# Performance work log

Hardware: AMD Instinct MI355X
Metric: run time of the kernel (lower is better)

Reference implementation:

```python
import jax, jax.numpy as jnp
import numpy as np

DROPOUT_P = 0.5  # used as an additive constant in the normalizers, not as dropout
N = 384


def setup_inputs() -> dict:
    key = jax.random.key(0)
    k1, k2 = jax.random.split(key)
    inp = jax.random.uniform(k1, (N, N, N), dtype=jnp.float32)
    w = jax.random.uniform(k2, (N, N, N), dtype=jnp.float32)
    return {"input": inp, "w": w}


def reference(input, w):
    # e[i,j,l] = sum_k input[i,j,k] * w[l,k,j]
    e = jnp.einsum('ijk,lkj->ijl', input, w)
    # k (normalized by input row-sums) is dead code in the original forward;
    # only q and v feed the output, so we skip it.
    v = e  # second identical einsum in the source
    s_in = input.sum(axis=-1, keepdims=True)          # [N, N, 1]
    # einsum('ijk,ijl->ijl', input, w) == (sum_k input) * w
    q = s_in * w
    q = q / (DROPOUT_P + w.sum(axis=-1, keepdims=True))
    # causal mask: strict upper triangle set to -inf, broadcast over batch
    mask = jnp.triu(jnp.full((N, N), -jnp.inf, dtype=q.dtype), k=1)  # [N, N]
    attn = jax.nn.softmax(q + mask[None, :, :], axis=-1)              # [N, N, N]
    return jnp.matmul(attn, v)
```

## Files before the change

### kernel.cpp

```cpp
#include <hip/hip_runtime.h>
#include <hip/hip_bf16.h>


#define N 384
#define N2 (N * N)
#define BK 64
static const size_t N3 = (size_t)N * N * N;

typedef __attribute__((ext_vector_type(8))) short s16x8;
typedef __attribute__((ext_vector_type(4))) float f32x4;

#define AS1 __attribute__((address_space(1)))
#define AS3 __attribute__((address_space(3)))
__device__ __forceinline__ void gll16(const void* g, void* l) {
    __builtin_amdgcn_global_load_lds((const AS1 unsigned int*)g,
                                     (AS3 unsigned int*)l, 16, 0, 0);
}

__device__ __forceinline__ unsigned short f32_to_bf16(float f) {
    unsigned int u = __float_as_uint(f);
    u += 0x7FFFu + ((u >> 16) & 1u);
    return (unsigned short)(u >> 16);
}
__device__ __forceinline__ float bf16_to_f32(unsigned short h) {
    return __uint_as_float((unsigned int)h << 16);
}
__device__ __forceinline__ unsigned int pk2(float a, float b) {
    return (unsigned int)f32_to_bf16(a) | ((unsigned int)f32_to_bf16(b) << 16);
}

__global__ __launch_bounds__(256) void kT(const float* __restrict__ w,
                                          unsigned short* __restrict__ wt) {
    __shared__ unsigned short tile[64][68];
    const int r0 = blockIdx.x * 64;
    const int j0 = blockIdx.y * 64;
    const int tx = threadIdx.x & 63;
    const int ty = threadIdx.x >> 6;
#pragma unroll
    for (int p = 0; p < 16; ++p) {
        const int r = ty * 16 + p;
        tile[r][tx] = f32_to_bf16(w[(size_t)(r0 + r) * N + j0 + tx]);
    }
    __syncthreads();
#pragma unroll
    for (int p = 0; p < 16; ++p) {
        const int jj = ty * 16 + p;
        wt[(size_t)(j0 + jj) * N2 + r0 + tx] = tile[tx][jj];
    }
}

__global__ __launch_bounds__(256, 4) void k_e2(const float* __restrict__ in,
                                               const unsigned short* __restrict__ wt,
                                               unsigned short* __restrict__ e,
                                               float* __restrict__ rs) {
    __shared__ union {
        struct { unsigned short A[64 * 64]; unsigned short B[192 * 64]; } s;
        unsigned short C[64 * 200];
    } sm;

    const int lin = blockIdx.x;
    const int swz = (lin & 7) * 576 + (lin >> 3);
    const int j   = swz / 12;
    const int sub = swz % 12;
    const int i0  = (sub >> 1) * 64;
    const int l0  = (sub & 1) * 192;

    const int t = threadIdx.x, lane = t & 63, wv = t >> 6;
    const int fr = lane & 15, fx = lane >> 4;

    const int ra = t >> 2, ca = (t & 3) * 2;
    const float* Ab = in + (size_t)(i0 + ra) * N2 + (size_t)j * N + ca * 8;
    unsigned short* AsW0 = sm.s.A + ra * 64 + (((ca + 0) ^ (ra & 7)) * 8);
    unsigned short* AsW1 = sm.s.A + ra * 64 + (((ca + 1) ^ (ra & 7)) * 8);

    const unsigned short* Wj = wt + (size_t)j * N2 + (size_t)l0 * N;
    const int rb_off = lane >> 3;
    const int p8     = lane & 7;

    f32x4 acc[4][3];
#pragma unroll
    for (int m = 0; m < 4; ++m)
#pragma unroll
        for (int n = 0; n < 3; ++n) acc[m][n] = (f32x4){0.f, 0.f, 0.f, 0.f};

    float rsum = 0.f;

    float4 va[4];
    va[0] = *(const float4*)(Ab);
    va[1] = *(const float4*)(Ab + 4);
    va[2] = *(const float4*)(Ab + 8);
    va[3] = *(const float4*)(Ab + 12);

    for (int k0 = 0; k0 < N; k0 += BK) {
        __syncthreads();
        {
            rsum += (va[0].x + va[0].y + va[0].z + va[0].w) +
                    (va[1].x + va[1].y + va[1].z + va[1].w) +
                    (va[2].x + va[2].y + va[2].z + va[2].w) +
                    (va[3].x + va[3].y + va[3].z + va[3].w);
            uint4 a0, a1;
            a0.x = pk2(va[0].x, va[0].y); a0.y = pk2(va[0].z, va[0].w);
            a0.z = pk2(va[1].x, va[1].y); a0.w = pk2(va[1].z, va[1].w);
            a1.x = pk2(va[2].x, va[2].y); a1.y = pk2(va[2].z, va[2].w);
            a1.z = pk2(va[3].x, va[3].y); a1.w = pk2(va[3].z, va[3].w);
            *(uint4*)AsW0 = a0;
            *(uint4*)AsW1 = a1;
        }
#pragma unroll
        for (int itb = 0; itb < 6; ++itb) {
            const int rb = wv * 48 + itb * 8 + rb_off;
            const int sc = p8 ^ (rb & 7);
            gll16(Wj + (size_t)rb * N + k0 + sc * 8,
                  sm.s.B + (wv * 48 + itb * 8) * 64);
        }
        if (k0 + BK < N) {
            const float* An = Ab + k0 + BK;
            va[0] = *(const float4*)(An);
            va[1] = *(const float4*)(An + 4);
            va[2] = *(const float4*)(An + 8);
            va[3] = *(const float4*)(An + 12);
        }
        __syncthreads();
#pragma unroll
        for (int kk = 0; kk < 2; ++kk) {
            s16x8 af[4], bf[3];
#pragma unroll
            for (int m = 0; m < 4; ++m) {
                const int row = m * 16 + fr;
                const int x   = (kk * 4 + fx) ^ (row & 7);
                af[m] = *(const s16x8*)(sm.s.A + row * 64 + x * 8);
            }
#pragma unroll
            for (int n = 0; n < 3; ++n) {
                const int row = wv * 48 + n * 16 + fr;
                const int x   = (kk * 4 + fx) ^ (row & 7);
                bf[n] = *(const s16x8*)(sm.s.B + row * 64 + x * 8);
            }
#pragma unroll
            for (int m = 0; m < 4; ++m)
#pragma unroll
                for (int n = 0; n < 3; ++n)
                    acc[m][n] = __builtin_amdgcn_mfma_f32_16x16x32_bf16(
                        af[m], bf[n], acc[m][n], 0, 0, 0);
        }
    }

    rsum += __shfl_xor(rsum, 1, 64);
    rsum += __shfl_xor(rsum, 2, 64);
    if (rs != nullptr && l0 == 0 && (t & 3) == 0)
        rs[(size_t)(i0 + ra) * N + j] = rsum;

    __syncthreads();
#pragma unroll
    for (int m = 0; m < 4; ++m)
#pragma unroll
        for (int n = 0; n < 3; ++n)
#pragma unroll
            for (int r = 0; r < 4; ++r)
                sm.C[(m * 16 + fx * 4 + r) * 200 + wv * 48 + n * 16 + fr] =
                    f32_to_bf16(acc[m][n][r]);
    __syncthreads();
#pragma unroll
    for (int it = 0; it < 6; ++it) {
        const int cid = it * 256 + t;
        const int row = cid / 24;
        const int c   = cid % 24;
        *(uint4*)(e + (size_t)(i0 + row) * N2 + (size_t)j * N + l0 + c * 8) =
            *(const uint4*)&sm.C[row * 200 + c * 8];
    }
}

__global__ __launch_bounds__(256) void k_eT(const unsigned short* __restrict__ e,
                                            unsigned short* __restrict__ et) {
    __shared__ unsigned short tile[64][68];
    const int m0 = blockIdx.x * 64, l0 = blockIdx.y * 64;
    const size_t ib = (size_t)blockIdx.z * N2;
    const int t  = threadIdx.x;
    const int c4 = (t & 15) * 4, r = t >> 4;
#pragma unroll
    for (int p = 0; p < 4; ++p) {
        ushort4 v = *(const ushort4*)(e + ib + (size_t)(m0 + r + 16 * p) * N + l0 + c4);
        tile[c4 + 0][r + 16 * p] = v.x;
        tile[c4 + 1][r + 16 * p] = v.y;
        tile[c4 + 2][r + 16 * p] = v.z;
        tile[c4 + 3][r + 16 * p] = v.w;
    }
    __syncthreads();
#pragma unroll
    for (int p = 0; p < 4; ++p) {
        const int lr = r + 16 * p;
        ushort4 v = *(const ushort4*)&tile[lr][c4];
        *(ushort4*)(et + ib + (size_t)(l0 + lr) * N + m0 + c4) = v;
    }
}

template <bool HAVE_RS>
__global__ __launch_bounds__(256) void k_attn(const float* __restrict__ in,
                                              const float* __restrict__ w,
                                              const float* __restrict__ rs,
                                              unsigned short* __restrict__ attn) {
    const int row  = blockIdx.x * 4 + (threadIdx.x >> 6);
    const int lane = threadIdx.x & 63;
    const int jr   = row % N;

    const float2* wp = (const float2*)(w + (size_t)row * N);

    float2 wv[3];
    float rs_in = 0.f, rs_w = 0.f;
#pragma unroll
    for (int c = 0; c < 3; ++c) {
        wv[c] = wp[lane + 64 * c];
        rs_w += wv[c].x + wv[c].y;
    }
    if (HAVE_RS) {
#pragma unroll
        for (int s = 1; s < 64; s <<= 1) rs_w += __shfl_xor(rs_w, s, 64);
        rs_in = rs[row];
    } else {
        const float2* ip = (const float2*)(in + (size_t)row * N);
#pragma unroll
        for (int c = 0; c < 3; ++c) {
            float2 iv = ip[lane + 64 * c];
            rs_in += iv.x + iv.y;
        }
#pragma unroll
        for (int s = 1; s < 64; s <<= 1) {
            rs_in += __shfl_xor(rs_in, s, 64);
            rs_w  += __shfl_xor(rs_w, s, 64);
        }
    }
    const float scale = rs_in / (0.5f + rs_w);

    float2 q[3];
    float mx = -INFINITY;
#pragma unroll
    for (int c = 0; c < 3; ++c) {
        const int l = (lane + 64 * c) * 2;
        q[c].x = (l     <= jr) ? scale * wv[c].x : -INFINITY;
        q[c].y = (l + 1 <= jr) ? scale * wv[c].y : -INFINITY;
        mx = fmaxf(mx, fmaxf(q[c].x, q[c].y));
    }
#pragma unroll
    for (int s = 1; s < 64; s <<= 1) mx = fmaxf(mx, __shfl_xor(mx, s, 64));

    float2 p[3];
    float sum = 0.f;
#pragma unroll
    for (int c = 0; c < 3; ++c) {
        const int l = (lane + 64 * c) * 2;
        p[c].x = (l     <= jr) ? exp2f((q[c].x - mx) * 1.44269504f) : 0.f;
        p[c].y = (l + 1 <= jr) ? exp2f((q[c].y - mx) * 1.44269504f) : 0.f;
        sum += p[c].x + p[c].y;
    }
#pragma unroll
    for (int s = 1; s < 64; s <<= 1) sum += __shfl_xor(sum, s, 64);
    const float inv = 1.f / sum;
    unsigned int* ap = (unsigned int*)(attn + (size_t)row * N);
#pragma unroll
    for (int c = 0; c < 3; ++c)
        ap[lane + 64 * c] = pk2(p[c].x * inv, p[c].y * inv);
}

__global__ __launch_bounds__(256, 4) void k_av2(const unsigned short* __restrict__ attn,
                                                const unsigned short* __restrict__ et,
                                                float* __restrict__ out) {
    __shared__ union {
        struct { unsigned short A[64 * 64]; unsigned short B[192 * 64]; } s;
        float C[32 * 196];
    } sm;

    const int lin = blockIdx.x;
    const int swz = (lin & 7) * 576 + (lin >> 3);
    const int i   = swz / 12;
    const int sub = swz % 12;
    const int j0  = (sub >> 1) * 64;
    const int l0  = (sub & 1) * 192;
    const int kmax = j0 + 64;

    const int t = threadIdx.x, lane = t & 63, wv = t >> 6;
    const int fr = lane & 15, fx = lane >> 4;
    const int rb_off = lane >> 3;
    const int p8     = lane & 7;

    const unsigned short* Ag = attn + (size_t)i * N2 + (size_t)j0 * N;
    const unsigned short* Bg = et + (size_t)i * N2 + (size_t)l0 * N;

    f32x4 acc[4][3];
#pragma unroll
    for (int m = 0; m < 4; ++m)
#pragma unroll
        for (int n = 0; n < 3; ++n) acc[m][n] = (f32x4){0.f, 0.f, 0.f, 0.f};

    for (int k0 = 0; k0 < kmax; k0 += BK) {
        __syncthreads();
#pragma unroll
        for (int ita = 0; ita < 2; ++ita) {
            const int rb = wv * 16 + ita * 8 + rb_off;
            const int sc = p8 ^ (rb & 7);
            gll16(Ag + (size_t)rb * N + k0 + sc * 8,
                  sm.s.A + (wv * 16 + ita * 8) * 64);
        }
#pragma unroll
        for (int itb = 0; itb < 6; ++itb) {
            const int rb = wv * 48 + itb * 8 + rb_off;
            const int sc = p8 ^ (rb & 7);
            gll16(Bg + (size_t)rb * N + k0 + sc * 8,
                  sm.s.B + (wv * 48 + itb * 8) * 64);
        }
        __syncthreads();
#pragma unroll
        for (int kk = 0; kk < 2; ++kk) {
            s16x8 af[4], bf[3];
#pragma unroll
            for (int m = 0; m < 4; ++m) {
                const int row = m * 16 + fr;
                const int x   = (kk * 4 + fx) ^ (row & 7);
                af[m] = *(const s16x8*)(sm.s.A + row * 64 + x * 8);
            }
#pragma unroll
            for (int n = 0; n < 3; ++n) {
                const int row = wv * 48 + n * 16 + fr;
                const int x   = (kk * 4 + fx) ^ (row & 7);
                bf[n] = *(const s16x8*)(sm.s.B + row * 64 + x * 8);
            }
#pragma unroll
            for (int m = 0; m < 4; ++m)
#pragma unroll
                for (int n = 0; n < 3; ++n)
                    acc[m][n] = __builtin_amdgcn_mfma_f32_16x16x32_bf16(
                        af[m], bf[n], acc[m][n], 0, 0, 0);
        }
    }

#pragma unroll
    for (int ph = 0; ph < 2; ++ph) {
        __syncthreads();
#pragma unroll
        for (int mm = 0; mm < 2; ++mm)
#pragma unroll
            for (int n = 0; n < 3; ++n)
#pragma unroll
                for (int r = 0; r < 4; ++r)
                    sm.C[(mm * 16 + fx * 4 + r) * 196 + wv * 48 + n * 16 + fr] =
                        acc[ph * 2 + mm][n][r];
        __syncthreads();
#pragma unroll
        for (int it = 0; it < 6; ++it) {
            const int cid = it * 256 + t;
            const int row = cid / 48;
            const int c   = cid % 48;
            *(float4*)(out + (size_t)i * N2 + (size_t)(j0 + ph * 32 + row) * N + l0 + c * 4) =
                *(const float4*)&sm.C[row * 196 + c * 4];
        }
    }
}

extern "C" void kernel_launch(void* const* d_in, const int* in_sizes, int n_in,
                              void* d_out, int out_size, void* d_ws, size_t ws_size,
                              hipStream_t stream) {
    const float* in = (const float*)d_in[0];
    const float* w  = (const float*)d_in[1];
    float* out      = (float*)d_out;

    unsigned short* r0 = (unsigned short*)d_ws;
    unsigned short* r1 = (unsigned short*)d_ws + N3;
    const bool have_rs = ws_size >= 2 * N3 * sizeof(unsigned short) + (size_t)N2 * sizeof(float);
    float* rs = have_rs ? (float*)((unsigned short*)d_ws + 2 * N3) : nullptr;

    kT<<<dim3(N2 / 64, N / 64), 256, 0, stream>>>(w, r0);
    k_e2<<<dim3(4608), 256, 0, stream>>>(in, r0, r1, rs);
    k_eT<<<dim3(6, 6, N), 256, 0, stream>>>(r1, r0);
    if (have_rs)
        k_attn<true><<<dim3(N2 / 4), 256, 0, stream>>>(in, w, rs, r1);
    else
        k_attn<false><<<dim3(N2 / 4), 256, 0, stream>>>(in, w, nullptr, r1);
    k_av2<<<dim3(4608), 256, 0, stream>>>(r1, r0, out);
}
```

Measured before the change: 398.5 us.

## Double-buffer LDS tiles in e and attn·v GEMM kernels with manual waitcnt

Both the e-projection and the attn·v GEMM kernels now keep two LDS buffers for the A and B tiles. The global-to-LDS loads for the next K tile are issued before the MFMA work on the current tile, with explicit vmcnt/lgkmcnt waits and raw barriers in place of __syncthreads, and the MFMA section is wrapped in s_setprio. This aims to hide global load latency behind compute. The cost is double the LDS per block, so launch bounds drop from 4 to 2 blocks per SM, which lowers occupancy. The hand-written waitcnt counts are fragile.

Result: slower. 412.1 us (+3.4%).

```diff
diff --git a/kernel.cpp b/kernel.cpp
--- a/kernel.cpp
+++ b/kernel.cpp
@@ -16,6 +16,10 @@
     __builtin_amdgcn_global_load_lds((const AS1 unsigned int*)g,
                                      (AS3 unsigned int*)l, 16, 0, 0);
 }
+#define WAITV4 asm volatile("s_waitcnt vmcnt(4)" ::: "memory")
+#define WAITV0 asm volatile("s_waitcnt vmcnt(0)" ::: "memory")
+#define WAITL0 asm volatile("s_waitcnt lgkmcnt(0)" ::: "memory")
+#define BAR    __builtin_amdgcn_s_barrier()
 
 __device__ __forceinline__ unsigned short f32_to_bf16(float f) {
     unsigned int u = __float_as_uint(f);
@@ -49,12 +53,12 @@
     }
 }
 
-__global__ __launch_bounds__(256, 4) void k_e2(const float* __restrict__ in,
+__global__ __launch_bounds__(256, 2) void k_e2(const float* __restrict__ in,
                                                const unsigned short* __restrict__ wt,
                                                unsigned short* __restrict__ e,
                                                float* __restrict__ rs) {
     __shared__ union {
-        struct { unsigned short A[64 * 64]; unsigned short B[192 * 64]; } s;
+        struct { unsigned short A[2][64 * 64]; unsigned short B[2][192 * 64]; } s;
         unsigned short C[64 * 200];
     } sm;
 
@@ -70,8 +74,8 @@
 
     const int ra = t >> 2, ca = (t & 3) * 2;
     const float* Ab = in + (size_t)(i0 + ra) * N2 + (size_t)j * N + ca * 8;
-    unsigned short* AsW0 = sm.s.A + ra * 64 + (((ca + 0) ^ (ra & 7)) * 8);
-    unsigned short* AsW1 = sm.s.A + ra * 64 + (((ca + 1) ^ (ra & 7)) * 8);
+    const int aswz0 = ra * 64 + (((ca + 0) ^ (ra & 7)) * 8);
+    const int aswz1 = ra * 64 + (((ca + 1) ^ (ra & 7)) * 8);
 
     const unsigned short* Wj = wt + (size_t)j * N2 + (size_t)l0 * N;
     const int rb_off = lane >> 3;
@@ -84,16 +88,53 @@
         for (int n = 0; n < 3; ++n) acc[m][n] = (f32x4){0.f, 0.f, 0.f, 0.f};
 
     float rsum = 0.f;
-
     float4 va[4];
+
     va[0] = *(const float4*)(Ab);
     va[1] = *(const float4*)(Ab + 4);
     va[2] = *(const float4*)(Ab + 8);
     va[3] = *(const float4*)(Ab + 12);
-
-    for (int k0 = 0; k0 < N; k0 += BK) {
-        __syncthreads();
-        {
+#pragma unroll
+    for (int itb = 0; itb < 6; ++itb) {
+        const int rb = wv * 48 + itb * 8 + rb_off;
+        const int sc = p8 ^ (rb & 7);
+        gll16(Wj + (size_t)rb * N + sc * 8, sm.s.B[0] + (wv * 48 + itb * 8) * 64);
+    }
+    {
+        rsum += (va[0].x + va[0].y + va[0].z + va[0].w) +
+                (va[1].x + va[1].y + va[1].z + va[1].w) +
+                (va[2].x + va[2].y + va[2].z + va[2].w) +
+                (va[3].x + va[3].y + va[3].z + va[3].w);
+        uint4 a0, a1;
+        a0.x = pk2(va[0].x, va[0].y); a0.y = pk2(va[0].z, va[0].w);
+        a0.z = pk2(va[1].x, va[1].y); a0.w = pk2(va[1].z, va[1].w);
+        a1.x = pk2(va[2].x, va[2].y); a1.y = pk2(va[2].z, va[2].w);
+        a1.z = pk2(va[3].x, va[3].y); a1.w = pk2(va[3].z, va[3].w);
+        *(uint4*)(sm.s.A[0] + aswz0) = a0;
+        *(uint4*)(sm.s.A[0] + aswz1) = a1;
+    }
+    va[0] = *(const float4*)(Ab + 64);
+    va[1] = *(const float4*)(Ab + 68);
+    va[2] = *(const float4*)(Ab + 72);
+    va[3] = *(const float4*)(Ab + 76);
+    WAITV4;
+    WAITL0;
+    BAR;
+
+#pragma unroll
+    for (int tt = 0; tt < 6; ++tt) {
+        unsigned short* Ac = sm.s.A[tt & 1];
+        unsigned short* An = sm.s.A[(tt + 1) & 1];
+        unsigned short* Bc = sm.s.B[tt & 1];
+        unsigned short* Bn = sm.s.B[(tt + 1) & 1];
+        if (tt < 5) {
+            const int kn = (tt + 1) * 64;
+#pragma unroll
+            for (int itb = 0; itb < 6; ++itb) {
+                const int rb = wv * 48 + itb * 8 + rb_off;
+                const int sc = p8 ^ (rb & 7);
+                gll16(Wj + (size_t)rb * N + kn + sc * 8, Bn + (wv * 48 + itb * 8) * 64);
+            }
             rsum += (va[0].x + va[0].y + va[0].z + va[0].w) +
                     (va[1].x + va[1].y + va[1].z + va[1].w) +
                     (va[2].x + va[2].y + va[2].z + va[2].w) +
@@ -103,24 +144,17 @@
             a0.z = pk2(va[1].x, va[1].y); a0.w = pk2(va[1].z, va[1].w);
             a1.x = pk2(va[2].x, va[2].y); a1.y = pk2(va[2].z, va[2].w);
             a1.z = pk2(va[3].x, va[3].y); a1.w = pk2(va[3].z, va[3].w);
-            *(uint4*)AsW0 = a0;
-            *(uint4*)AsW1 = a1;
-        }
-#pragma unroll
-        for (int itb = 0; itb < 6; ++itb) {
-            const int rb = wv * 48 + itb * 8 + rb_off;
-            const int sc = p8 ^ (rb & 7);
-            gll16(Wj + (size_t)rb * N + k0 + sc * 8,
-                  sm.s.B + (wv * 48 + itb * 8) * 64);
-        }
-        if (k0 + BK < N) {
-            const float* An = Ab + k0 + BK;
-            va[0] = *(const float4*)(An);
-            va[1] = *(const float4*)(An + 4);
-            va[2] = *(const float4*)(An + 8);
-            va[3] = *(const float4*)(An + 12);
-        }
-        __syncthreads();
+            *(uint4*)(An + aswz0) = a0;
+            *(uint4*)(An + aswz1) = a1;
+        }
+        if (tt < 4) {
+            const float* Axn = Ab + (tt + 2) * 64;
+            va[0] = *(const float4*)(Axn);
+            va[1] = *(const float4*)(Axn + 4);
+            va[2] = *(const float4*)(Axn + 8);
+            va[3] = *(const float4*)(Axn + 12);
+        }
+        __builtin_amdgcn_s_setprio(1);
 #pragma unroll
         for (int kk = 0; kk < 2; ++kk) {
             s16x8 af[4], bf[3];
@@ -128,13 +162,13 @@
             for (int m = 0; m < 4; ++m) {
                 const int row = m * 16 + fr;
                 const int x   = (kk * 4 + fx) ^ (row & 7);
-                af[m] = *(const s16x8*)(sm.s.A + row * 64 + x * 8);
+                af[m] = *(const s16x8*)(Ac + row * 64 + x * 8);
             }
 #pragma unroll
             for (int n = 0; n < 3; ++n) {
                 const int row = wv * 48 + n * 16 + fr;
                 const int x   = (kk * 4 + fx) ^ (row & 7);
-                bf[n] = *(const s16x8*)(sm.s.B + row * 64 + x * 8);
+                bf[n] = *(const s16x8*)(Bc + row * 64 + x * 8);
             }
 #pragma unroll
             for (int m = 0; m < 4; ++m)
@@ -142,6 +176,12 @@
                 for (int n = 0; n < 3; ++n)
                     acc[m][n] = __builtin_amdgcn_mfma_f32_16x16x32_bf16(
                         af[m], bf[n], acc[m][n], 0, 0, 0);
+        }
+        __builtin_amdgcn_s_setprio(0);
+        if (tt < 5) {
+            if (tt < 4) { WAITV4; } else { WAITV0; }
+            WAITL0;
+            BAR;
         }
     }
 
@@ -261,11 +301,11 @@
         ap[lane + 64 * c] = pk2(p[c].x * inv, p[c].y * inv);
 }
 
-__global__ __launch_bounds__(256, 4) void k_av2(const unsigned short* __restrict__ attn,
+__global__ __launch_bounds__(256, 2) void k_av2(const unsigned short* __restrict__ attn,
                                                 const unsigned short* __restrict__ et,
                                                 float* __restrict__ out) {
     __shared__ union {
-        struct { unsigned short A[64 * 64]; unsigned short B[192 * 64]; } s;
+        struct { unsigned short A[2][64 * 64]; unsigned short B[2][192 * 64]; } s;
         float C[32 * 196];
     } sm;
 
@@ -275,7 +315,7 @@
     const int sub = swz % 12;
     const int j0  = (sub >> 1) * 64;
     const int l0  = (sub & 1) * 192;
-    const int kmax = j0 + 64;
+    const int nt  = (j0 >> 6) + 1;
 
     const int t = threadIdx.x, lane = t & 63, wv = t >> 6;
     const int fr = lane & 15, fx = lane >> 4;
@@ -291,23 +331,43 @@
 #pragma unroll
         for (int n = 0; n < 3; ++n) acc[m][n] = (f32x4){0.f, 0.f, 0.f, 0.f};
 
-    for (int k0 = 0; k0 < kmax; k0 += BK) {
-        __syncthreads();
-#pragma unroll
-        for (int ita = 0; ita < 2; ++ita) {
-            const int rb = wv * 16 + ita * 8 + rb_off;
-            const int sc = p8 ^ (rb & 7);
-            gll16(Ag + (size_t)rb * N + k0 + sc * 8,
-                  sm.s.A + (wv * 16 + ita * 8) * 64);
-        }
-#pragma unroll
-        for (int itb = 0; itb < 6; ++itb) {
-            const int rb = wv * 48 + itb * 8 + rb_off;
-            const int sc = p8 ^ (rb & 7);
-            gll16(Bg + (size_t)rb * N + k0 + sc * 8,
-                  sm.s.B + (wv * 48 + itb * 8) * 64);
-        }
-        __syncthreads();
+    unsigned short* Ac = sm.s.A[0];
+    unsigned short* An = sm.s.A[1];
+    unsigned short* Bc = sm.s.B[0];
+    unsigned short* Bn = sm.s.B[1];
+
+#pragma unroll
+    for (int ita = 0; ita < 2; ++ita) {
+        const int rb = wv * 16 + ita * 8 + rb_off;
+        const int sc = p8 ^ (rb & 7);
+        gll16(Ag + (size_t)rb * N + sc * 8, Ac + (wv * 16 + ita * 8) * 64);
+    }
+#pragma unroll
+    for (int itb = 0; itb < 6; ++itb) {
+        const int rb = wv * 48 + itb * 8 + rb_off;
+        const int sc = p8 ^ (rb & 7);
+        gll16(Bg + (size_t)rb * N + sc * 8, Bc + (wv * 48 + itb * 8) * 64);
+    }
+    WAITV0;
+    BAR;
+
+    for (int tt = 0; tt < nt; ++tt) {
+        if (tt + 1 < nt) {
+            const int kn = (tt + 1) * 64;
+#pragma unroll
+            for (int ita = 0; ita < 2; ++ita) {
+                const int rb = wv * 16 + ita * 8 + rb_off;
+                const int sc = p8 ^ (rb & 7);
+                gll16(Ag + (size_t)rb * N + kn + sc * 8, An + (wv * 16 + ita * 8) * 64);
+            }
+#pragma unroll
+            for (int itb = 0; itb < 6; ++itb) {
+                const int rb = wv * 48 + itb * 8 + rb_off;
+                const int sc = p8 ^ (rb & 7);
+                gll16(Bg + (size_t)rb * N + kn + sc * 8, Bn + (wv * 48 + itb * 8) * 64);
+            }
+        }
+        __builtin_amdgcn_s_setprio(1);
 #pragma unroll
         for (int kk = 0; kk < 2; ++kk) {
             s16x8 af[4], bf[3];
@@ -315,13 +375,13 @@
             for (int m = 0; m < 4; ++m) {
                 const int row = m * 16 + fr;
                 const int x   = (kk * 4 + fx) ^ (row & 7);
-                af[m] = *(const s16x8*)(sm.s.A + row * 64 + x * 8);
+                af[m] = *(const s16x8*)(Ac + row * 64 + x * 8);
             }
 #pragma unroll
             for (int n = 0; n < 3; ++n) {
                 const int row = wv * 48 + n * 16 + fr;
                 const int x   = (kk * 4 + fx) ^ (row & 7);
-                bf[n] = *(const s16x8*)(sm.s.B + row * 64 + x * 8);
+                bf[n] = *(const s16x8*)(Bc + row * 64 + x * 8);
             }
 #pragma unroll
             for (int m = 0; m < 4; ++m)
@@ -330,11 +390,19 @@
                     acc[m][n] = __builtin_amdgcn_mfma_f32_16x16x32_bf16(
                         af[m], bf[n], acc[m][n], 0, 0, 0);
         }
-    }
-
+        __builtin_amdgcn_s_setprio(0);
+        if (tt + 1 < nt) {
+            WAITV0;
+            BAR;
+            unsigned short* tp;
+            tp = Ac; Ac = An; An = tp;
+            tp = Bc; Bc = Bn; Bn = tp;
+        }
+    }
+
+    __syncthreads();
 #pragma unroll
     for (int ph = 0; ph < 2; ++ph) {
-        __syncthreads();
 #pragma unroll
         for (int mm = 0; mm < 2; ++mm)
 #pragma unroll
@@ -352,6 +420,7 @@
             *(float4*)(out + (size_t)i * N2 + (size_t)(j0 + ph * 32 + row) * N + l0 + c * 4) =
                 *(const float4*)&sm.C[row * 196 + c * 4];
         }
+        if (ph == 0) __syncthreads();
     }
 }
 
```

## Fuse causal softmax into attention-value matmul, computing probabilities on the fly

Applied to the files above, without the earlier changes.

Removes the separate softmax kernel that wrote a bf16 attention matrix. The matmul kernel now computes the row max and sum from w and the row sums, then builds the bf16 probability tiles directly into LDS for each k-tile. This cuts the write and re-read of a full N^3 bf16 tensor and one kernel launch. In exchange, w rows are read again by each of the two l-halves, exponentials are recomputed redundantly, and register pressure rises.

Result: slower. 425.2 us (+6.7%).

```diff
diff --git a/kernel.cpp b/kernel.cpp
--- a/kernel.cpp
+++ b/kernel.cpp
@@ -21,9 +21,6 @@
     unsigned int u = __float_as_uint(f);
     u += 0x7FFFu + ((u >> 16) & 1u);
     return (unsigned short)(u >> 16);
-}
-__device__ __forceinline__ float bf16_to_f32(unsigned short h) {
-    return __uint_as_float((unsigned int)h << 16);
 }
 __device__ __forceinline__ unsigned int pk2(float a, float b) {
     return (unsigned int)f32_to_bf16(a) | ((unsigned int)f32_to_bf16(b) << 16);
@@ -195,73 +192,9 @@
 }
 
 template <bool HAVE_RS>
-__global__ __launch_bounds__(256) void k_attn(const float* __restrict__ in,
-                                              const float* __restrict__ w,
-                                              const float* __restrict__ rs,
-                                              unsigned short* __restrict__ attn) {
-    const int row  = blockIdx.x * 4 + (threadIdx.x >> 6);
-    const int lane = threadIdx.x & 63;
-    const int jr   = row % N;
-
-    const float2* wp = (const float2*)(w + (size_t)row * N);
-
-    float2 wv[3];
-    float rs_in = 0.f, rs_w = 0.f;
-#pragma unroll
-    for (int c = 0; c < 3; ++c) {
-        wv[c] = wp[lane + 64 * c];
-        rs_w += wv[c].x + wv[c].y;
-    }
-    if (HAVE_RS) {
-#pragma unroll
-        for (int s = 1; s < 64; s <<= 1) rs_w += __shfl_xor(rs_w, s, 64);
-        rs_in = rs[row];
-    } else {
-        const float2* ip = (const float2*)(in + (size_t)row * N);
-#pragma unroll
-        for (int c = 0; c < 3; ++c) {
-            float2 iv = ip[lane + 64 * c];
-            rs_in += iv.x + iv.y;
-        }
-#pragma unroll
-        for (int s = 1; s < 64; s <<= 1) {
-            rs_in += __shfl_xor(rs_in, s, 64);
-            rs_w  += __shfl_xor(rs_w, s, 64);
-        }
-    }
-    const float scale = rs_in / (0.5f + rs_w);
-
-    float2 q[3];
-    float mx = -INFINITY;
-#pragma unroll
-    for (int c = 0; c < 3; ++c) {
-        const int l = (lane + 64 * c) * 2;
-        q[c].x = (l     <= jr) ? scale * wv[c].x : -INFINITY;
-        q[c].y = (l + 1 <= jr) ? scale * wv[c].y : -INFINITY;
-        mx = fmaxf(mx, fmaxf(q[c].x, q[c].y));
-    }
-#pragma unroll
-    for (int s = 1; s < 64; s <<= 1) mx = fmaxf(mx, __shfl_xor(mx, s, 64));
-
-    float2 p[3];
-    float sum = 0.f;
-#pragma unroll
-    for (int c = 0; c < 3; ++c) {
-        const int l = (lane + 64 * c) * 2;
-        p[c].x = (l     <= jr) ? exp2f((q[c].x - mx) * 1.44269504f) : 0.f;
-        p[c].y = (l + 1 <= jr) ? exp2f((q[c].y - mx) * 1.44269504f) : 0.f;
-        sum += p[c].x + p[c].y;
-    }
-#pragma unroll
-    for (int s = 1; s < 64; s <<= 1) sum += __shfl_xor(sum, s, 64);
-    const float inv = 1.f / sum;
-    unsigned int* ap = (unsigned int*)(attn + (size_t)row * N);
-#pragma unroll
-    for (int c = 0; c < 3; ++c)
-        ap[lane + 64 * c] = pk2(p[c].x * inv, p[c].y * inv);
-}
-
-__global__ __launch_bounds__(256, 4) void k_av2(const unsigned short* __restrict__ attn,
+__global__ __launch_bounds__(256, 4) void k_av3(const float* __restrict__ in,
+                                                const float* __restrict__ w,
+                                                const float* __restrict__ rs,
                                                 const unsigned short* __restrict__ et,
                                                 float* __restrict__ out) {
     __shared__ union {
@@ -275,14 +208,68 @@
     const int sub = swz % 12;
     const int j0  = (sub >> 1) * 64;
     const int l0  = (sub & 1) * 192;
-    const int kmax = j0 + 64;
+    const int nt  = (j0 >> 6) + 1;
 
     const int t = threadIdx.x, lane = t & 63, wv = t >> 6;
     const int fr = lane & 15, fx = lane >> 4;
     const int rb_off = lane >> 3;
     const int p8     = lane & 7;
 
-    const unsigned short* Ag = attn + (size_t)i * N2 + (size_t)j0 * N;
+    const int ra = t >> 2;
+    const int q0 = t & 3;
+    const int jrow = j0 + ra;
+    const float* Wrow = w + (size_t)i * N2 + (size_t)jrow * N;
+
+    float s_w = 0.f, mx = -INFINITY;
+    float rs_in = 0.f;
+#pragma unroll
+    for (int c = 0; c < 24; ++c) {
+        const int col = q0 * 4 + c * 16;
+        float4 v = *(const float4*)(Wrow + col);
+        s_w += v.x + v.y + v.z + v.w;
+        float m0 = (col + 0 <= jrow) ? v.x : -INFINITY;
+        float m1 = (col + 1 <= jrow) ? v.y : -INFINITY;
+        float m2 = (col + 2 <= jrow) ? v.z : -INFINITY;
+        float m3 = (col + 3 <= jrow) ? v.w : -INFINITY;
+        mx = fmaxf(mx, fmaxf(fmaxf(m0, m1), fmaxf(m2, m3)));
+    }
+    if (!HAVE_RS) {
+        const float* Irow = in + (size_t)i * N2 + (size_t)jrow * N;
+#pragma unroll
+        for (int c = 0; c < 24; ++c) {
+            float4 v = *(const float4*)(Irow + q0 * 4 + c * 16);
+            rs_in += v.x + v.y + v.z + v.w;
+        }
+        rs_in += __shfl_xor(rs_in, 1, 64);
+        rs_in += __shfl_xor(rs_in, 2, 64);
+    }
+    s_w += __shfl_xor(s_w, 1, 64);
+    s_w += __shfl_xor(s_w, 2, 64);
+    mx = fmaxf(mx, __shfl_xor(mx, 1, 64));
+    mx = fmaxf(mx, __shfl_xor(mx, 2, 64));
+    if (HAVE_RS) rs_in = rs[(size_t)i * N + jrow];
+
+    const float scale = rs_in / (0.5f + s_w);
+    const float aa = scale * 1.44269504f;
+
+    float s_e = 0.f;
+#pragma unroll
+    for (int c = 0; c < 24; ++c) {
+        const int col = q0 * 4 + c * 16;
+        float4 v = *(const float4*)(Wrow + col);
+        float e0 = (col + 0 <= jrow) ? exp2f(aa * (v.x - mx)) : 0.f;
+        float e1 = (col + 1 <= jrow) ? exp2f(aa * (v.y - mx)) : 0.f;
+        float e2 = (col + 2 <= jrow) ? exp2f(aa * (v.z - mx)) : 0.f;
+        float e3 = (col + 3 <= jrow) ? exp2f(aa * (v.w - mx)) : 0.f;
+        s_e += e0 + e1 + e2 + e3;
+    }
+    s_e += __shfl_xor(s_e, 1, 64);
+    s_e += __shfl_xor(s_e, 2, 64);
+    const float nb = -(aa * mx + __log2f(s_e));
+
+    unsigned short* AsW0 = sm.s.A + ra * 64 + (((q0 * 2 + 0) ^ (ra & 7)) * 8);
+    unsigned short* AsW1 = sm.s.A + ra * 64 + (((q0 * 2 + 1) ^ (ra & 7)) * 8);
+    const float* Ab = Wrow + q0 * 16;
     const unsigned short* Bg = et + (size_t)i * N2 + (size_t)l0 * N;
 
     f32x4 acc[4][3];
@@ -291,14 +278,32 @@
 #pragma unroll
         for (int n = 0; n < 3; ++n) acc[m][n] = (f32x4){0.f, 0.f, 0.f, 0.f};
 
-    for (int k0 = 0; k0 < kmax; k0 += BK) {
-        __syncthreads();
-#pragma unroll
-        for (int ita = 0; ita < 2; ++ita) {
-            const int rb = wv * 16 + ita * 8 + rb_off;
-            const int sc = p8 ^ (rb & 7);
-            gll16(Ag + (size_t)rb * N + k0 + sc * 8,
-                  sm.s.A + (wv * 16 + ita * 8) * 64);
+    float4 va[4];
+    va[0] = *(const float4*)(Ab);
+    va[1] = *(const float4*)(Ab + 4);
+    va[2] = *(const float4*)(Ab + 8);
+    va[3] = *(const float4*)(Ab + 12);
+
+    for (int tt = 0; tt < nt; ++tt) {
+        const int k0 = tt * 64;
+        __syncthreads();
+        {
+            const int lim = jrow - k0 - q0 * 16;
+            float p[16];
+#pragma unroll
+            for (int f = 0; f < 4; ++f) {
+                p[f * 4 + 0] = (f * 4 + 0 <= lim) ? exp2f(fmaf(aa, va[f].x, nb)) : 0.f;
+                p[f * 4 + 1] = (f * 4 + 1 <= lim) ? exp2f(fmaf(aa, va[f].y, nb)) : 0.f;
+                p[f * 4 + 2] = (f * 4 + 2 <= lim) ? exp2f(fmaf(aa, va[f].z, nb)) : 0.f;
+                p[f * 4 + 3] = (f * 4 + 3 <= lim) ? exp2f(fmaf(aa, va[f].w, nb)) : 0.f;
+            }
+            uint4 a0, a1;
+            a0.x = pk2(p[0], p[1]);   a0.y = pk2(p[2], p[3]);
+            a0.z = pk2(p[4], p[5]);   a0.w = pk2(p[6], p[7]);
+            a1.x = pk2(p[8], p[9]);   a1.y = pk2(p[10], p[11]);
+            a1.z = pk2(p[12], p[13]); a1.w = pk2(p[14], p[15]);
+            *(uint4*)AsW0 = a0;
+            *(uint4*)AsW1 = a1;
         }
 #pragma unroll
         for (int itb = 0; itb < 6; ++itb) {
@@ -307,6 +312,13 @@
             gll16(Bg + (size_t)rb * N + k0 + sc * 8,
                   sm.s.B + (wv * 48 + itb * 8) * 64);
         }
+        if (tt + 1 < nt) {
+            const float* An = Ab + k0 + 64;
+            va[0] = *(const float4*)(An);
+            va[1] = *(const float4*)(An + 4);
+            va[2] = *(const float4*)(An + 8);
+            va[3] = *(const float4*)(An + 12);
+        }
         __syncthreads();
 #pragma unroll
         for (int kk = 0; kk < 2; ++kk) {
@@ -332,9 +344,9 @@
         }
     }
 
+    __syncthreads();
 #pragma unroll
     for (int ph = 0; ph < 2; ++ph) {
-        __syncthreads();
 #pragma unroll
         for (int mm = 0; mm < 2; ++mm)
 #pragma unroll
@@ -352,6 +364,7 @@
             *(float4*)(out + (size_t)i * N2 + (size_t)(j0 + ph * 32 + row) * N + l0 + c * 4) =
                 *(const float4*)&sm.C[row * 196 + c * 4];
         }
+        if (ph == 0) __syncthreads();
     }
 }
 
@@ -371,8 +384,7 @@
     k_e2<<<dim3(4608), 256, 0, stream>>>(in, r0, r1, rs);
     k_eT<<<dim3(6, 6, N), 256, 0, stream>>>(r1, r0);
     if (have_rs)
-        k_attn<true><<<dim3(N2 / 4), 256, 0, stream>>>(in, w, rs, r1);
+        k_av3<true><<<dim3(4608), 256, 0, stream>>>(in, w, rs, r0, out);
     else
-        k_attn<false><<<dim3(N2 / 4), 256, 0, stream>>>(in, w, nullptr, r1);
-    k_av2<<<dim3(4608), 256, 0, stream>>>(r1, r0, out);
-}
+        k_av3<false><<<dim3(4608), 256, 0, stream>>>(in, w, nullptr, r0, out);
+}
```
